# Kernel optimization log

Measured on AMD Instinct MI355X. Metric: run time of the kernel, lower is better.

Reference implementation:

```python
import jax, jax.numpy as jnp
import numpy as np

N_NODES = 100000
N_EDGES = 1600000
N_FEAT = 128
NHID = 128
BATCH = 512


def gcn_conv(x, w, b, edge_index, edge_weight):
    """PyG GCNConv: symmetric-normalized aggregation with self-loops, then bias.
    edge_index[0]=source j, edge_index[1]=target i; out_i = sum_j norm_ij * (x_j @ W) + b.
    """
    n = x.shape[0]
    xw = x @ w  # [N, out]
    loop = jnp.arange(n)
    row = jnp.concatenate([edge_index[0], loop])  # sources
    col = jnp.concatenate([edge_index[1], loop])  # targets
    wts = jnp.concatenate([edge_weight, jnp.ones((n,), edge_weight.dtype)])
    deg = jax.ops.segment_sum(wts, col, num_segments=n)
    dinv = jnp.where(deg > 0, jax.lax.rsqrt(deg), jnp.zeros_like(deg))
    norm = dinv[row] * wts * dinv[col]  # [E+N]
    out = jax.ops.segment_sum(norm[:, None] * xw[row], col, num_segments=n)
    return out + b


def setup_inputs() -> dict:
    key = jax.random.key(0)
    ks = jax.random.split(key, 12)
    s = 1.0 / np.sqrt(NHID)
    return {
        "X": jax.random.normal(ks[0], (N_NODES, N_FEAT), jnp.float32),
        "edge_index": jax.random.randint(ks[1], (2, N_EDGES), 0, N_NODES, jnp.int64)
            if jax.config.jax_enable_x64 else jax.random.randint(ks[1], (2, N_EDGES), 0, N_NODES, jnp.int32),
        "edge_weight": jax.random.uniform(ks[2], (N_EDGES,), jnp.float32),
        "batch_vec": jnp.sort(jax.random.randint(ks[3], (N_NODES,), 0, BATCH, jnp.int32)),
        "W1": jax.random.normal(ks[4], (N_FEAT, NHID), jnp.float32) * s,
        "b1": jnp.zeros((NHID,), jnp.float32),
        "W2": jax.random.normal(ks[5], (NHID, NHID), jnp.float32) * s,
        "b2": jnp.zeros((NHID,), jnp.float32),
        "W3": jax.random.normal(ks[6], (NHID, NHID), jnp.float32) * s,
        "b3": jnp.zeros((NHID,), jnp.float32),
        "lin_w": jax.random.normal(ks[7], (NHID, 1), jnp.float32) * s,
        "lin_b": jnp.zeros((1,), jnp.float32),
    }


def reference(X, edge_index, edge_weight, batch_vec, W1, b1, W2, b2, W3, b3, lin_w, lin_b):
    x = jax.nn.relu(gcn_conv(X, W1, b1, edge_index, edge_weight))
    # dropout is identity in eval mode
    x = jax.nn.relu(gcn_conv(x, W2, b2, edge_index, edge_weight))
    x = jax.nn.relu(gcn_conv(x, W3, b3, edge_index, edge_weight))
    # per-graph sum pooling (replaces the python torch.split loop)
    pooled = jax.ops.segment_sum(x, batch_vec, num_segments=BATCH)  # [B, nhid3]
    out = pooled @ lin_w + lin_b  # [B, 1]
    return jnp.squeeze(out, axis=-1)  # [B]
```

## Files before the change

### kernel.cpp

```cpp
#include <hip/hip_runtime.h>
#include <hip/hip_fp16.h>

typedef __attribute__((ext_vector_type(8))) short bf16x8;
typedef __attribute__((ext_vector_type(4))) float f32x4;

#define CSR_PAD 64

__device__ __forceinline__ ushort f2bf(float f) {
  union { float f; uint u; } v; v.f = f;
  uint r = (v.u + 0x7fffu + ((v.u >> 16) & 1u)) >> 16;
  return (ushort)r;
}
__device__ __forceinline__ float2 bfp2f(uint p) {
  union { uint u; float f; } lo, hi;
  lo.u = p << 16; hi.u = p & 0xffff0000u;
  float2 r; r.x = lo.f; r.y = hi.f; return r;
}
__device__ __forceinline__ float u2f(uint u) {
  union { uint u; float f; } v; v.u = u; return v.f;
}
__device__ __forceinline__ float h15f(uint entry) {
  return u2f(((entry >> 17) << 13) + 0x38000000u);
}


__global__ void k_init(uint* cnt, float* pooled, int N, int pooledN) {
  int i = blockIdx.x * blockDim.x + threadIdx.x;
  if (i < N) cnt[i] = 0;
  if (i < pooledN) pooled[i] = 0.0f;
}


__global__ void k_wt3(const float* __restrict__ W1, const float* __restrict__ W2,
                      const float* __restrict__ W3, ushort* T1, ushort* T2, ushort* T3) {
  int which = blockIdx.x >> 6;
  const float* W = which == 0 ? W1 : (which == 1 ? W2 : W3);
  ushort* T = which == 0 ? T1 : (which == 1 ? T2 : T3);
  int idx = (blockIdx.x & 63) * 256 + threadIdx.x;
  int k = idx >> 7, c = idx & 127;
  T[c * 128 + k] = f2bf(W[idx]);
}


__global__ __launch_bounds__(256) void k_mega(
    const int* __restrict__ ei, const float* __restrict__ ew,
    uint* cnt, uint* csr, int E,
    const float* __restrict__ X, const ushort* __restrict__ Wt,
    ushort* __restrict__ C, int N, int gblocks) {
  int bid = blockIdx.x;
  int role_gemm, widx;
  if (bid < 2048) { role_gemm = bid & 1; widx = bid >> 1; }
  else            { role_gemm = 1;       widx = 1024 + (bid - 2048); }

  if (!role_gemm) {
    int stride = 1024 * 256;
    for (int e = widx * 256 + threadIdx.x; e < E; e += stride) {
      int src = ei[e];
      int dst = ei[E + e];
      float w = ew[e];
      uint pos = atomicAdd(&cnt[dst], 1u);
      if (pos < (uint)CSR_PAD) {
        union { __half h; ushort u; } cv; cv.h = __float2half(w);
        csr[((size_t)dst << 6) + pos] = (uint)src | ((uint)cv.u << 17);
      }
    }
    return;
  }

  if (widx >= gblocks) return;
  int wid = threadIdx.x >> 6, lane = threadIdx.x & 63;
  int row0 = widx * 64 + wid * 16;
  int r = lane & 15, kh = lane >> 4;
  int arow = row0 + r;
  bool inb = arow < N;
  bf16x8 afrag[4];
#pragma unroll
  for (int kc = 0; kc < 4; ++kc) {
    if (inb) {
      const float* p = &X[(size_t)arow * 128 + kc * 32 + kh * 8];
      float4 x0 = *(const float4*)p;
      float4 x1 = *(const float4*)(p + 4);
      bf16x8 t;
      t[0] = (short)f2bf(x0.x); t[1] = (short)f2bf(x0.y);
      t[2] = (short)f2bf(x0.z); t[3] = (short)f2bf(x0.w);
      t[4] = (short)f2bf(x1.x); t[5] = (short)f2bf(x1.y);
      t[6] = (short)f2bf(x1.z); t[7] = (short)f2bf(x1.w);
      afrag[kc] = t;
    } else {
      bf16x8 z = {0, 0, 0, 0, 0, 0, 0, 0};
      afrag[kc] = z;
    }
  }
  f32x4 acc[8];
#pragma unroll
  for (int ct = 0; ct < 8; ++ct) { f32x4 z = {0.f, 0.f, 0.f, 0.f}; acc[ct] = z; }
#pragma unroll
  for (int ct = 0; ct < 8; ++ct) {
#pragma unroll
    for (int kc = 0; kc < 4; ++kc) {
      bf16x8 b = *(const bf16x8*)&Wt[(size_t)(ct * 16 + r) * 128 + kc * 32 + kh * 8];
      acc[ct] = __builtin_amdgcn_mfma_f32_16x16x32_bf16(afrag[kc], b, acc[ct], 0, 0, 0);
    }
  }
#pragma unroll
  for (int rr = 0; rr < 4; ++rr) {
    int row = row0 + kh * 4 + rr;
    if (row < N) {
#pragma unroll
      for (int ct = 0; ct < 8; ++ct)
        C[(size_t)row * 128 + ct * 16 + r] = f2bf(acc[ct][rr]);
    }
  }
}


__global__ __launch_bounds__(256) void k_dinv_scale(const uint* __restrict__ csr,
                                                    uint* cnt, float* dinv,
                                                    ushort* y, int N) {
  int wid = threadIdx.x >> 6, lane = threadIdx.x & 63;
  int node = blockIdx.x * 4 + wid;
  if (node >= N) return;
  uint c = cnt[node];
  if (c > (uint)CSR_PAD) c = CSR_PAD;
  float w = ((uint)lane < c) ? h15f(csr[((size_t)node << 6) + lane]) : 0.f;
#pragma unroll
  for (int o = 32; o > 0; o >>= 1) w += __shfl_xor(w, o, 64);
  float di = rsqrtf(1.0f + w);
  if (lane == 0) { cnt[node] = c; dinv[node] = di; }
  uint p = *(const uint*)&y[(size_t)node * 128 + lane * 2];
  float2 f = bfp2f(p);
  ushort2 o2 = {f2bf(f.x * di), f2bf(f.y * di)};
  *(ushort2*)&y[(size_t)node * 128 + lane * 2] = o2;
}


__global__ __launch_bounds__(256) void k_gemm(const ushort* __restrict__ A,
                                              const ushort* __restrict__ Wt,
                                              const float* __restrict__ dinv,
                                              ushort* __restrict__ C, int N) {
  int wid = threadIdx.x >> 6, lane = threadIdx.x & 63;
  int row0 = blockIdx.x * 64 + wid * 16;
  int r = lane & 15, kh = lane >> 4;
  int arow = row0 + r;
  bool inb = arow < N;
  bf16x8 afrag[4];
#pragma unroll
  for (int kc = 0; kc < 4; ++kc) {
    if (inb) {
      afrag[kc] = *(const bf16x8*)&A[(size_t)arow * 128 + kc * 32 + kh * 8];
    } else {
      bf16x8 z = {0, 0, 0, 0, 0, 0, 0, 0};
      afrag[kc] = z;
    }
  }
  f32x4 acc[8];
#pragma unroll
  for (int ct = 0; ct < 8; ++ct) { f32x4 z = {0.f, 0.f, 0.f, 0.f}; acc[ct] = z; }
#pragma unroll
  for (int ct = 0; ct < 8; ++ct) {
#pragma unroll
    for (int kc = 0; kc < 4; ++kc) {
      bf16x8 b = *(const bf16x8*)&Wt[(size_t)(ct * 16 + r) * 128 + kc * 32 + kh * 8];
      acc[ct] = __builtin_amdgcn_mfma_f32_16x16x32_bf16(afrag[kc], b, acc[ct], 0, 0, 0);
    }
  }
#pragma unroll
  for (int rr = 0; rr < 4; ++rr) {
    int row = row0 + kh * 4 + rr;
    if (row < N) {
      float sc = dinv[row];
#pragma unroll
      for (int ct = 0; ct < 8; ++ct)
        C[(size_t)row * 128 + ct * 16 + r] = f2bf(acc[ct][rr] * sc);
    }
  }
}


__global__ __launch_bounds__(256) void k_agg(const ushort* __restrict__ y,
                                             const float* __restrict__ dinv,
                                             const uint* __restrict__ cnt,
                                             const uint* __restrict__ csr,
                                             const float* __restrict__ bias,
                                             ushort* __restrict__ out, int N) {
  int wid = threadIdx.x >> 6, lane = threadIdx.x & 63;
  int node = blockIdx.x * 4 + wid;
  if (node >= N) return;
  float di = dinv[node];
  uint selfp = *(const uint*)&y[(size_t)node * 128 + lane * 2];
  float2 sv = bfp2f(selfp);
  float2 a0 = {sv.x, sv.y};
  float2 a1 = {0.f, 0.f}, a2 = {0.f, 0.f}, a3 = {0.f, 0.f};
  int e = (int)cnt[node];
  const uint* cs = csr + ((size_t)node << 6);
  int i = 0;
  for (; i + 8 <= e; i += 8) {
    uint4 ca = *(const uint4*)&cs[i];
    uint4 cb = *(const uint4*)&cs[i + 4];
    uint g0 = *(const uint*)&y[(size_t)(ca.x & 0x1FFFFu) * 128 + lane * 2];
    uint g1 = *(const uint*)&y[(size_t)(ca.y & 0x1FFFFu) * 128 + lane * 2];
    uint g2 = *(const uint*)&y[(size_t)(ca.z & 0x1FFFFu) * 128 + lane * 2];
    uint g3 = *(const uint*)&y[(size_t)(ca.w & 0x1FFFFu) * 128 + lane * 2];
    uint g4 = *(const uint*)&y[(size_t)(cb.x & 0x1FFFFu) * 128 + lane * 2];
    uint g5 = *(const uint*)&y[(size_t)(cb.y & 0x1FFFFu) * 128 + lane * 2];
    uint g6 = *(const uint*)&y[(size_t)(cb.z & 0x1FFFFu) * 128 + lane * 2];
    uint g7 = *(const uint*)&y[(size_t)(cb.w & 0x1FFFFu) * 128 + lane * 2];
    float n0 = h15f(ca.x), n1 = h15f(ca.y), n2 = h15f(ca.z), n3 = h15f(ca.w);
    float n4 = h15f(cb.x), n5 = h15f(cb.y), n6 = h15f(cb.z), n7 = h15f(cb.w);
    float2 f0 = bfp2f(g0), f1 = bfp2f(g1), f2 = bfp2f(g2), f3 = bfp2f(g3);
    float2 f4 = bfp2f(g4), f5 = bfp2f(g5), f6 = bfp2f(g6), f7 = bfp2f(g7);
    a0.x = fmaf(n0, f0.x, a0.x); a0.y = fmaf(n0, f0.y, a0.y);
    a1.x = fmaf(n1, f1.x, a1.x); a1.y = fmaf(n1, f1.y, a1.y);
    a2.x = fmaf(n2, f2.x, a2.x); a2.y = fmaf(n2, f2.y, a2.y);
    a3.x = fmaf(n3, f3.x, a3.x); a3.y = fmaf(n3, f3.y, a3.y);
    a0.x = fmaf(n4, f4.x, a0.x); a0.y = fmaf(n4, f4.y, a0.y);
    a1.x = fmaf(n5, f5.x, a1.x); a1.y = fmaf(n5, f5.y, a1.y);
    a2.x = fmaf(n6, f6.x, a2.x); a2.y = fmaf(n6, f6.y, a2.y);
    a3.x = fmaf(n7, f7.x, a3.x); a3.y = fmaf(n7, f7.y, a3.y);
  }
  for (; i + 4 <= e; i += 4) {
    uint4 ca = *(const uint4*)&cs[i];
    uint g0 = *(const uint*)&y[(size_t)(ca.x & 0x1FFFFu) * 128 + lane * 2];
    uint g1 = *(const uint*)&y[(size_t)(ca.y & 0x1FFFFu) * 128 + lane * 2];
    uint g2 = *(const uint*)&y[(size_t)(ca.z & 0x1FFFFu) * 128 + lane * 2];
    uint g3 = *(const uint*)&y[(size_t)(ca.w & 0x1FFFFu) * 128 + lane * 2];
    float n0 = h15f(ca.x), n1 = h15f(ca.y), n2 = h15f(ca.z), n3 = h15f(ca.w);
    float2 f0 = bfp2f(g0), f1 = bfp2f(g1), f2 = bfp2f(g2), f3 = bfp2f(g3);
    a0.x = fmaf(n0, f0.x, a0.x); a0.y = fmaf(n0, f0.y, a0.y);
    a1.x = fmaf(n1, f1.x, a1.x); a1.y = fmaf(n1, f1.y, a1.y);
    a2.x = fmaf(n2, f2.x, a2.x); a2.y = fmaf(n2, f2.y, a2.y);
    a3.x = fmaf(n3, f3.x, a3.x); a3.y = fmaf(n3, f3.y, a3.y);
  }
  for (; i < e; ++i) {
    uint c0 = cs[i];
    uint g0 = *(const uint*)&y[(size_t)(c0 & 0x1FFFFu) * 128 + lane * 2];
    float n0 = h15f(c0);
    float2 f0 = bfp2f(g0);
    a0.x = fmaf(n0, f0.x, a0.x); a0.y = fmaf(n0, f0.y, a0.y);
  }
  float bx = bias[lane * 2], by = bias[lane * 2 + 1];
  float rx = fmaxf(fmaf(di, a0.x + a1.x + a2.x + a3.x, bx), 0.f);
  float ry = fmaxf(fmaf(di, a0.y + a1.y + a2.y + a3.y, by), 0.f);
  ushort2 o = {f2bf(rx), f2bf(ry)};
  *(ushort2*)&out[(size_t)node * 128 + lane * 2] = o;
}


__global__ __launch_bounds__(256) void k_pool(const ushort* __restrict__ x,
                                              const int* __restrict__ batch,
                                              float* pooled, int N) {
  int wid = threadIdx.x >> 6, lane = threadIdx.x & 63;
  int n0 = (blockIdx.x * 4 + wid) * 32;
  if (n0 >= N) return;
  int n1 = min(n0 + 32, N);
  int cur = batch[n0];
  float ax = 0.f, ay = 0.f;
  for (int n = n0; n < n1; ++n) {
    int b = batch[n];
    if (b != cur) {
      atomicAdd(&pooled[cur * 128 + lane * 2], ax);
      atomicAdd(&pooled[cur * 128 + lane * 2 + 1], ay);
      ax = 0.f; ay = 0.f;
      cur = b;
    }
    uint p = *(const uint*)&x[(size_t)n * 128 + lane * 2];
    float2 f = bfp2f(p);
    ax += f.x; ay += f.y;
  }
  atomicAdd(&pooled[cur * 128 + lane * 2], ax);
  atomicAdd(&pooled[cur * 128 + lane * 2 + 1], ay);
}

__global__ void k_final(const float* __restrict__ pooled, const float* __restrict__ lw,
                        const float* __restrict__ lb, float* __restrict__ out) {
  int b = blockIdx.x;
  int l = threadIdx.x;
  float s = pooled[b * 128 + l] * lw[l] + pooled[b * 128 + 64 + l] * lw[64 + l];
#pragma unroll
  for (int o = 32; o > 0; o >>= 1) s += __shfl_down(s, o, 64);
  if (l == 0) out[b] = s + lb[0];
}


extern "C" void kernel_launch(void* const* d_in, const int* in_sizes, int n_in,
                              void* d_out, int out_size, void* d_ws, size_t ws_size,
                              hipStream_t stream) {
  const float* X  = (const float*)d_in[0];
  const int*   ei = (const int*)d_in[1];
  const float* ew = (const float*)d_in[2];
  const int*   bv = (const int*)d_in[3];
  const float* W1 = (const float*)d_in[4];
  const float* b1 = (const float*)d_in[5];
  const float* W2 = (const float*)d_in[6];
  const float* b2 = (const float*)d_in[7];
  const float* W3 = (const float*)d_in[8];
  const float* b3 = (const float*)d_in[9];
  const float* lw = (const float*)d_in[10];
  const float* lb = (const float*)d_in[11];
  float* out = (float*)d_out;

  int N = in_sizes[0] / 128;
  int E = in_sizes[2];
  int B = out_size;

  char* wsp = (char*)d_ws;
  size_t off = 0;
  auto alloc = [&](size_t bytes) -> void* {
    void* p = wsp + off;
    off += (bytes + 255) & ~(size_t)255;
    return p;
  };
  uint*   cnt      = (uint*)alloc((size_t)N * 4);
  float*  dinv     = (float*)alloc((size_t)N * 4);
  uint*   csr      = (uint*)alloc((size_t)N * CSR_PAD * 4);
  ushort* wt1      = (ushort*)alloc(128 * 128 * 2);
  ushort* wt2      = (ushort*)alloc(128 * 128 * 2);
  ushort* wt3      = (ushort*)alloc(128 * 128 * 2);
  ushort* buf0     = (ushort*)alloc((size_t)N * 128 * 2);
  ushort* buf1     = (ushort*)alloc((size_t)N * 128 * 2);
  float*  pooled   = (float*)alloc((size_t)B * 128 * 4);
  (void)ws_size; (void)n_in;

  int nthr = 256;
  int nb_n = (N + nthr - 1) / nthr;
  int nb_w = (N + 3) / 4;
  int gblocks = (N + 63) / 64;

  k_init<<<nb_n, nthr, 0, stream>>>(cnt, pooled, N, B * 128);
  k_wt3<<<192, 256, 0, stream>>>(W1, W2, W3, wt1, wt2, wt3);
  k_mega<<<1024 + gblocks, 256, 0, stream>>>(ei, ew, cnt, csr, E,
                                             X, wt1, buf0, N, gblocks);
  k_dinv_scale<<<nb_w, 256, 0, stream>>>(csr, cnt, dinv, buf0, N);

  k_agg<<<nb_w, 256, 0, stream>>>(buf0, dinv, cnt, csr, b1, buf1, N);
  k_gemm<<<gblocks, 256, 0, stream>>>(buf1, wt2, dinv, buf0, N);
  k_agg<<<nb_w, 256, 0, stream>>>(buf0, dinv, cnt, csr, b2, buf1, N);
  k_gemm<<<gblocks, 256, 0, stream>>>(buf1, wt3, dinv, buf0, N);
  k_agg<<<nb_w, 256, 0, stream>>>(buf0, dinv, cnt, csr, b3, buf1, N);

  int pblocks = (N + 127) / 128;
  k_pool<<<pblocks, 256, 0, stream>>>(buf1, bv, pooled, N);
  k_final<<<B, 64, 0, stream>>>(pooled, lw, lb, out);
}
```

Baseline: 396.6 us.

## Sort per-node CSR neighbours by source index and stage GEMM weights in LDS

The prep kernel now bitonic-sorts each node's padded neighbour list by source-node index with wave shuffles. It records boundaries at quarter-ranges of the index space so the aggregation walks neighbours in ascending address order, aiming at better cache and TLB locality of the gathers across the three layers. The GEMM kernel also copies the transposed weight matrix into shared memory once per block instead of reading it from global memory per fragment. This adds sort cost once, a 32KB LDS footprint per GEMM block, and more loop-tail overhead from splitting aggregation into four segments.

Result: slower. 451.2 us (+13.8%).

```diff
diff --git a/kernel.cpp b/kernel.cpp
--- a/kernel.cpp
+++ b/kernel.cpp
@@ -114,19 +114,46 @@
 }
 
 
-__global__ __launch_bounds__(256) void k_dinv_scale(const uint* __restrict__ csr,
-                                                    uint* cnt, float* dinv,
-                                                    ushort* y, int N) {
+__global__ __launch_bounds__(256) void k_prep(uint* csr, uint* cnt, float* dinv,
+                                              uchar4* bnd, ushort* y, int N) {
   int wid = threadIdx.x >> 6, lane = threadIdx.x & 63;
   int node = blockIdx.x * 4 + wid;
   if (node >= N) return;
   uint c = cnt[node];
   if (c > (uint)CSR_PAD) c = CSR_PAD;
-  float w = ((uint)lane < c) ? h15f(csr[((size_t)node << 6) + lane]) : 0.f;
-#pragma unroll
-  for (int o = 32; o > 0; o >>= 1) w += __shfl_xor(w, o, 64);
-  float di = rsqrtf(1.0f + w);
-  if (lane == 0) { cnt[node] = c; dinv[node] = di; }
+  uint entry = ((uint)lane < c) ? csr[((size_t)node << 6) + lane] : 0xFFFFFFFFu;
+  float w = ((uint)lane < c) ? h15f(entry) : 0.f;
+  float ws = w;
+#pragma unroll
+  for (int o = 32; o > 0; o >>= 1) ws += __shfl_xor(ws, o, 64);
+  float di = rsqrtf(1.0f + ws);
+  uint t = ((uint)lane < c) ? ((entry << 15) | (entry >> 17)) : 0xFFFFFFFFu;
+#pragma unroll
+  for (int k = 2; k <= 64; k <<= 1) {
+#pragma unroll
+    for (int j = k >> 1; j > 0; j >>= 1) {
+      uint p = (uint)__shfl_xor((int)t, j, 64);
+      bool up = ((lane & k) == 0);
+      bool keepmin = (((lane & j) == 0) == up);
+      uint mn = min(t, p), mx = max(t, p);
+      t = keepmin ? mn : mx;
+    }
+  }
+  unsigned long long m1 = __ballot(t < (1u << 30));
+  unsigned long long m2 = __ballot(t < (2u << 30));
+  unsigned long long m3 = __ballot(t < (3u << 30));
+  if ((uint)lane < c)
+    csr[((size_t)node << 6) + lane] = (t >> 15) | (t << 17);
+  if (lane == 0) {
+    uchar4 b;
+    b.x = (unsigned char)__popcll(m1);
+    b.y = (unsigned char)__popcll(m2);
+    b.z = (unsigned char)__popcll(m3);
+    b.w = (unsigned char)c;
+    bnd[node] = b;
+    cnt[node] = c;
+    dinv[node] = di;
+  }
   uint p = *(const uint*)&y[(size_t)node * 128 + lane * 2];
   float2 f = bfp2f(p);
   ushort2 o2 = {f2bf(f.x * di), f2bf(f.y * di)};
@@ -138,7 +165,17 @@
                                               const ushort* __restrict__ Wt,
                                               const float* __restrict__ dinv,
                                               ushort* __restrict__ C, int N) {
-  int wid = threadIdx.x >> 6, lane = threadIdx.x & 63;
+  __shared__ ushort wlds[128 * 128];
+  int tid = threadIdx.x;
+  {
+    const uint4* src = (const uint4*)Wt;
+    uint4* dst = (uint4*)wlds;
+#pragma unroll
+    for (int j = 0; j < 8; ++j) dst[tid + 256 * j] = src[tid + 256 * j];
+  }
+  __syncthreads();
+
+  int wid = tid >> 6, lane = tid & 63;
   int row0 = blockIdx.x * 64 + wid * 16;
   int r = lane & 15, kh = lane >> 4;
   int arow = row0 + r;
@@ -160,7 +197,7 @@
   for (int ct = 0; ct < 8; ++ct) {
 #pragma unroll
     for (int kc = 0; kc < 4; ++kc) {
-      bf16x8 b = *(const bf16x8*)&Wt[(size_t)(ct * 16 + r) * 128 + kc * 32 + kh * 8];
+      bf16x8 b = *(const bf16x8*)&wlds[(ct * 16 + r) * 128 + kc * 32 + kh * 8];
       acc[ct] = __builtin_amdgcn_mfma_f32_16x16x32_bf16(afrag[kc], b, acc[ct], 0, 0, 0);
     }
   }
@@ -179,7 +216,7 @@
 
 __global__ __launch_bounds__(256) void k_agg(const ushort* __restrict__ y,
                                              const float* __restrict__ dinv,
-                                             const uint* __restrict__ cnt,
+                                             const uchar4* __restrict__ bnd,
                                              const uint* __restrict__ csr,
                                              const float* __restrict__ bias,
                                              ushort* __restrict__ out, int N) {
@@ -191,53 +228,61 @@
   float2 sv = bfp2f(selfp);
   float2 a0 = {sv.x, sv.y};
   float2 a1 = {0.f, 0.f}, a2 = {0.f, 0.f}, a3 = {0.f, 0.f};
-  int e = (int)cnt[node];
   const uint* cs = csr + ((size_t)node << 6);
-  int i = 0;
-  for (; i + 8 <= e; i += 8) {
-    uint4 ca = *(const uint4*)&cs[i];
-    uint4 cb = *(const uint4*)&cs[i + 4];
-    uint g0 = *(const uint*)&y[(size_t)(ca.x & 0x1FFFFu) * 128 + lane * 2];
-    uint g1 = *(const uint*)&y[(size_t)(ca.y & 0x1FFFFu) * 128 + lane * 2];
-    uint g2 = *(const uint*)&y[(size_t)(ca.z & 0x1FFFFu) * 128 + lane * 2];
-    uint g3 = *(const uint*)&y[(size_t)(ca.w & 0x1FFFFu) * 128 + lane * 2];
-    uint g4 = *(const uint*)&y[(size_t)(cb.x & 0x1FFFFu) * 128 + lane * 2];
-    uint g5 = *(const uint*)&y[(size_t)(cb.y & 0x1FFFFu) * 128 + lane * 2];
-    uint g6 = *(const uint*)&y[(size_t)(cb.z & 0x1FFFFu) * 128 + lane * 2];
-    uint g7 = *(const uint*)&y[(size_t)(cb.w & 0x1FFFFu) * 128 + lane * 2];
-    float n0 = h15f(ca.x), n1 = h15f(ca.y), n2 = h15f(ca.z), n3 = h15f(ca.w);
-    float n4 = h15f(cb.x), n5 = h15f(cb.y), n6 = h15f(cb.z), n7 = h15f(cb.w);
-    float2 f0 = bfp2f(g0), f1 = bfp2f(g1), f2 = bfp2f(g2), f3 = bfp2f(g3);
-    float2 f4 = bfp2f(g4), f5 = bfp2f(g5), f6 = bfp2f(g6), f7 = bfp2f(g7);
-    a0.x = fmaf(n0, f0.x, a0.x); a0.y = fmaf(n0, f0.y, a0.y);
-    a1.x = fmaf(n1, f1.x, a1.x); a1.y = fmaf(n1, f1.y, a1.y);
-    a2.x = fmaf(n2, f2.x, a2.x); a2.y = fmaf(n2, f2.y, a2.y);
-    a3.x = fmaf(n3, f3.x, a3.x); a3.y = fmaf(n3, f3.y, a3.y);
-    a0.x = fmaf(n4, f4.x, a0.x); a0.y = fmaf(n4, f4.y, a0.y);
-    a1.x = fmaf(n5, f5.x, a1.x); a1.y = fmaf(n5, f5.y, a1.y);
-    a2.x = fmaf(n6, f6.x, a2.x); a2.y = fmaf(n6, f6.y, a2.y);
-    a3.x = fmaf(n7, f7.x, a3.x); a3.y = fmaf(n7, f7.y, a3.y);
-  }
-  for (; i + 4 <= e; i += 4) {
-    uint4 ca = *(const uint4*)&cs[i];
-    uint g0 = *(const uint*)&y[(size_t)(ca.x & 0x1FFFFu) * 128 + lane * 2];
-    uint g1 = *(const uint*)&y[(size_t)(ca.y & 0x1FFFFu) * 128 + lane * 2];
-    uint g2 = *(const uint*)&y[(size_t)(ca.z & 0x1FFFFu) * 128 + lane * 2];
-    uint g3 = *(const uint*)&y[(size_t)(ca.w & 0x1FFFFu) * 128 + lane * 2];
-    float n0 = h15f(ca.x), n1 = h15f(ca.y), n2 = h15f(ca.z), n3 = h15f(ca.w);
-    float2 f0 = bfp2f(g0), f1 = bfp2f(g1), f2 = bfp2f(g2), f3 = bfp2f(g3);
-    a0.x = fmaf(n0, f0.x, a0.x); a0.y = fmaf(n0, f0.y, a0.y);
-    a1.x = fmaf(n1, f1.x, a1.x); a1.y = fmaf(n1, f1.y, a1.y);
-    a2.x = fmaf(n2, f2.x, a2.x); a2.y = fmaf(n2, f2.y, a2.y);
-    a3.x = fmaf(n3, f3.x, a3.x); a3.y = fmaf(n3, f3.y, a3.y);
-  }
-  for (; i < e; ++i) {
-    uint c0 = cs[i];
-    uint g0 = *(const uint*)&y[(size_t)(c0 & 0x1FFFFu) * 128 + lane * 2];
-    float n0 = h15f(c0);
-    float2 f0 = bfp2f(g0);
-    a0.x = fmaf(n0, f0.x, a0.x); a0.y = fmaf(n0, f0.y, a0.y);
-  }
+  uchar4 b = bnd[node];
+
+  auto process = [&](int i, int e) {
+    for (; i + 8 <= e; i += 8) {
+      uint c0 = cs[i],     c1 = cs[i + 1], c2 = cs[i + 2], c3 = cs[i + 3];
+      uint c4 = cs[i + 4], c5 = cs[i + 5], c6 = cs[i + 6], c7 = cs[i + 7];
+      uint g0 = *(const uint*)&y[(size_t)(c0 & 0x1FFFFu) * 128 + lane * 2];
+      uint g1 = *(const uint*)&y[(size_t)(c1 & 0x1FFFFu) * 128 + lane * 2];
+      uint g2 = *(const uint*)&y[(size_t)(c2 & 0x1FFFFu) * 128 + lane * 2];
+      uint g3 = *(const uint*)&y[(size_t)(c3 & 0x1FFFFu) * 128 + lane * 2];
+      uint g4 = *(const uint*)&y[(size_t)(c4 & 0x1FFFFu) * 128 + lane * 2];
+      uint g5 = *(const uint*)&y[(size_t)(c5 & 0x1FFFFu) * 128 + lane * 2];
+      uint g6 = *(const uint*)&y[(size_t)(c6 & 0x1FFFFu) * 128 + lane * 2];
+      uint g7 = *(const uint*)&y[(size_t)(c7 & 0x1FFFFu) * 128 + lane * 2];
+      float n0 = h15f(c0), n1 = h15f(c1), n2 = h15f(c2), n3 = h15f(c3);
+      float n4 = h15f(c4), n5 = h15f(c5), n6 = h15f(c6), n7 = h15f(c7);
+      float2 f0 = bfp2f(g0), f1 = bfp2f(g1), f2 = bfp2f(g2), f3 = bfp2f(g3);
+      float2 f4 = bfp2f(g4), f5 = bfp2f(g5), f6 = bfp2f(g6), f7 = bfp2f(g7);
+      a0.x = fmaf(n0, f0.x, a0.x); a0.y = fmaf(n0, f0.y, a0.y);
+      a1.x = fmaf(n1, f1.x, a1.x); a1.y = fmaf(n1, f1.y, a1.y);
+      a2.x = fmaf(n2, f2.x, a2.x); a2.y = fmaf(n2, f2.y, a2.y);
+      a3.x = fmaf(n3, f3.x, a3.x); a3.y = fmaf(n3, f3.y, a3.y);
+      a0.x = fmaf(n4, f4.x, a0.x); a0.y = fmaf(n4, f4.y, a0.y);
+      a1.x = fmaf(n5, f5.x, a1.x); a1.y = fmaf(n5, f5.y, a1.y);
+      a2.x = fmaf(n6, f6.x, a2.x); a2.y = fmaf(n6, f6.y, a2.y);
+      a3.x = fmaf(n7, f7.x, a3.x); a3.y = fmaf(n7, f7.y, a3.y);
+    }
+    for (; i + 4 <= e; i += 4) {
+      uint c0 = cs[i], c1 = cs[i + 1], c2 = cs[i + 2], c3 = cs[i + 3];
+      uint g0 = *(const uint*)&y[(size_t)(c0 & 0x1FFFFu) * 128 + lane * 2];
+      uint g1 = *(const uint*)&y[(size_t)(c1 & 0x1FFFFu) * 128 + lane * 2];
+      uint g2 = *(const uint*)&y[(size_t)(c2 & 0x1FFFFu) * 128 + lane * 2];
+      uint g3 = *(const uint*)&y[(size_t)(c3 & 0x1FFFFu) * 128 + lane * 2];
+      float n0 = h15f(c0), n1 = h15f(c1), n2 = h15f(c2), n3 = h15f(c3);
+      float2 f0 = bfp2f(g0), f1 = bfp2f(g1), f2 = bfp2f(g2), f3 = bfp2f(g3);
+      a0.x = fmaf(n0, f0.x, a0.x); a0.y = fmaf(n0, f0.y, a0.y);
+      a1.x = fmaf(n1, f1.x, a1.x); a1.y = fmaf(n1, f1.y, a1.y);
+      a2.x = fmaf(n2, f2.x, a2.x); a2.y = fmaf(n2, f2.y, a2.y);
+      a3.x = fmaf(n3, f3.x, a3.x); a3.y = fmaf(n3, f3.y, a3.y);
+    }
+    for (; i < e; ++i) {
+      uint c0 = cs[i];
+      uint g0 = *(const uint*)&y[(size_t)(c0 & 0x1FFFFu) * 128 + lane * 2];
+      float n0 = h15f(c0);
+      float2 f0 = bfp2f(g0);
+      a0.x = fmaf(n0, f0.x, a0.x); a0.y = fmaf(n0, f0.y, a0.y);
+    }
+  };
+
+  process(0, b.x);
+  process(b.x, b.y);
+  process(b.y, b.z);
+  process(b.z, b.w);
+
   float bx = bias[lane * 2], by = bias[lane * 2 + 1];
   float rx = fmaxf(fmaf(di, a0.x + a1.x + a2.x + a3.x, bx), 0.f);
   float ry = fmaxf(fmaf(di, a0.y + a1.y + a2.y + a3.y, by), 0.f);
@@ -313,6 +358,7 @@
   uint*   cnt      = (uint*)alloc((size_t)N * 4);
   float*  dinv     = (float*)alloc((size_t)N * 4);
   uint*   csr      = (uint*)alloc((size_t)N * CSR_PAD * 4);
+  uchar4* bnd      = (uchar4*)alloc((size_t)N * 4);
   ushort* wt1      = (ushort*)alloc(128 * 128 * 2);
   ushort* wt2      = (ushort*)alloc(128 * 128 * 2);
   ushort* wt3      = (ushort*)alloc(128 * 128 * 2);
@@ -330,13 +376,13 @@
   k_wt3<<<192, 256, 0, stream>>>(W1, W2, W3, wt1, wt2, wt3);
   k_mega<<<1024 + gblocks, 256, 0, stream>>>(ei, ew, cnt, csr, E,
                                              X, wt1, buf0, N, gblocks);
-  k_dinv_scale<<<nb_w, 256, 0, stream>>>(csr, cnt, dinv, buf0, N);
-
-  k_agg<<<nb_w, 256, 0, stream>>>(buf0, dinv, cnt, csr, b1, buf1, N);
+  k_prep<<<nb_w, 256, 0, stream>>>(csr, cnt, dinv, bnd, buf0, N);
+
+  k_agg<<<nb_w, 256, 0, stream>>>(buf0, dinv, bnd, csr, b1, buf1, N);
   k_gemm<<<gblocks, 256, 0, stream>>>(buf1, wt2, dinv, buf0, N);
-  k_agg<<<nb_w, 256, 0, stream>>>(buf0, dinv, cnt, csr, b2, buf1, N);
+  k_agg<<<nb_w, 256, 0, stream>>>(buf0, dinv, bnd, csr, b2, buf1, N);
   k_gemm<<<gblocks, 256, 0, stream>>>(buf1, wt3, dinv, buf0, N);
-  k_agg<<<nb_w, 256, 0, stream>>>(buf0, dinv, cnt, csr, b3, buf1, N);
+  k_agg<<<nb_w, 256, 0, stream>>>(buf0, dinv, bnd, csr, b3, buf1, N);
 
   int pblocks = (N + 127) / 128;
   k_pool<<<pblocks, 256, 0, stream>>>(buf1, bv, pooled, N);
```
